# Kernel optimization log

Hardware: AMD Instinct MI355X
Metric: run time of the kernel (lower is better)

Reference implementation:

```python
import jax, jax.numpy as jnp
import numpy as np

N = 50000
E = 800000
IN_FEATS = 128
OUT_FEATS = 64
ALPHA = 0.2  # LeakyReLU negative slope


def setup_inputs() -> dict:
    key = jax.random.key(0)
    k1, k2, k3, k4, k5 = jax.random.split(key, 5)
    h = jax.random.normal(k1, (N, IN_FEATS), dtype=jnp.float32)
    src = jax.random.randint(k2, (E,), 0, N)
    dst = jax.random.randint(k3, (E,), 0, N)
    edge_index = jnp.stack([src, dst], axis=0).astype(jnp.int64)
    # xavier_uniform with gain=1.414
    limW = 1.414 * np.sqrt(6.0 / (IN_FEATS + OUT_FEATS))
    W = jax.random.uniform(k4, (IN_FEATS, OUT_FEATS), dtype=jnp.float32, minval=-limW, maxval=limW)
    lima = 1.414 * np.sqrt(6.0 / (2 * OUT_FEATS + 1))
    a = jax.random.uniform(k5, (2 * OUT_FEATS, 1), dtype=jnp.float32, minval=-lima, maxval=lima)
    return {"h": h, "edge_index": edge_index, "W": W, "a": a}


def reference(h, edge_index, W, a):
    src, dst = edge_index[0], edge_index[1]
    Wh = h @ W                               # (N, out)
    # split attention vector: cat([Wh_src, Wh_dst]) @ a == Wh_src@a1 + Wh_dst@a2
    a1 = a[:OUT_FEATS, 0]                    # (out,)
    a2 = a[OUT_FEATS:, 0]                    # (out,)
    s1 = Wh @ a1                             # (N,)
    s2 = Wh @ a2                             # (N,)
    e = jax.nn.leaky_relu(s1[src] + s2[dst], negative_slope=ALPHA)  # (E,)
    exp_e = jnp.exp(e)
    denom = jax.ops.segment_sum(exp_e, dst, num_segments=N)          # (N,)
    attention = exp_e / denom[dst]                                   # (E,)
    # dropout p=0.0 / eval mode -> identity
    msgs = attention[:, None] * Wh[src]                              # (E, out)
    h_prime = jax.ops.segment_sum(msgs, dst, num_segments=N)         # (N, out)
    return jax.nn.elu(h_prime)
```

## Files before the change

### kernel.cpp

```cpp
#include <hip/hip_runtime.h>
#include <math.h>

#define GN 50000
#define GE 800000
#define INF 128
#define OUTF 64
#define LRELU_ALPHA 0.2f

#define BUCK_SH 6
#define BUCKW   64
#define NB      ((GN + BUCKW - 1) / BUCKW)
#define CHUNK   4096
#define NCH     ((GE + CHUNK - 1) / CHUNK)
#define CAP     1536

__device__ __forceinline__ unsigned short f32_to_bf16(float f) {
    unsigned int u = __float_as_uint(f);
    return (unsigned short)((u + 0x7fffu + ((u >> 16) & 1u)) >> 16);
}
__device__ __forceinline__ float bf16lo(unsigned int u) { return __uint_as_float(u << 16); }
__device__ __forceinline__ float bf16hi(unsigned int u) { return __uint_as_float(u & 0xffff0000u); }

__global__ __launch_bounds__(256) void k_front(const float* __restrict__ h,
                                               const float* __restrict__ W,
                                               const float* __restrict__ a,
                                               const int* __restrict__ src,
                                               const int* __restrict__ dst,
                                               unsigned short* __restrict__ Whb,
                                               float* __restrict__ s1,
                                               float* __restrict__ s2,
                                               int* __restrict__ ccount,
                                               int* __restrict__ epacked) {
    __shared__ __align__(16) float Wlds[INF * OUTF];
    int t = threadIdx.x;

    if (blockIdx.x < NB) {
        for (int i = t * 4; i < INF * OUTF; i += 256 * 4)
            *(float4*)&Wlds[i] = *(const float4*)&W[i];
        __syncthreads();

        int fg = t & 15;
        int ng = t >> 4;
        int jg = fg * 4;
        int n0 = blockIdx.x * 64 + ng * 4;

        int m0 = n0 + 0 < GN ? n0 + 0 : GN - 1;
        int m1 = n0 + 1 < GN ? n0 + 1 : GN - 1;
        int m2 = n0 + 2 < GN ? n0 + 2 : GN - 1;
        int m3 = n0 + 3 < GN ? n0 + 3 : GN - 1;
        const float* h0 = &h[m0 * INF];
        const float* h1 = &h[m1 * INF];
        const float* h2 = &h[m2 * INF];
        const float* h3 = &h[m3 * INF];

        float4 acc0 = {0.f,0.f,0.f,0.f}, acc1 = acc0, acc2 = acc0, acc3 = acc0;
        for (int kc = 0; kc < INF; kc += 4) {
            float4 hv0 = *(const float4*)&h0[kc];
            float4 hv1 = *(const float4*)&h1[kc];
            float4 hv2 = *(const float4*)&h2[kc];
            float4 hv3 = *(const float4*)&h3[kc];
            #pragma unroll
            for (int kk = 0; kk < 4; ++kk) {
                float4 wv = *(float4*)&Wlds[(kc + kk) * OUTF + jg];
                float a0 = ((const float*)&hv0)[kk];
                float a1v = ((const float*)&hv1)[kk];
                float a2v = ((const float*)&hv2)[kk];
                float a3 = ((const float*)&hv3)[kk];
                acc0.x += a0 * wv.x; acc0.y += a0 * wv.y; acc0.z += a0 * wv.z; acc0.w += a0 * wv.w;
                acc1.x += a1v * wv.x; acc1.y += a1v * wv.y; acc1.z += a1v * wv.z; acc1.w += a1v * wv.w;
                acc2.x += a2v * wv.x; acc2.y += a2v * wv.y; acc2.z += a2v * wv.z; acc2.w += a2v * wv.w;
                acc3.x += a3 * wv.x; acc3.y += a3 * wv.y; acc3.z += a3 * wv.z; acc3.w += a3 * wv.w;
            }
        }

        float4 accs[4] = {acc0, acc1, acc2, acc3};
        #pragma unroll
        for (int i = 0; i < 4; ++i) {
            if (n0 + i < GN) {
                ushort4 p;
                p.x = f32_to_bf16(accs[i].x); p.y = f32_to_bf16(accs[i].y);
                p.z = f32_to_bf16(accs[i].z); p.w = f32_to_bf16(accs[i].w);
                *(ushort4*)&Whb[(n0 + i) * OUTF + jg] = p;
            }
        }

        float4 va1 = *(const float4*)&a[jg];
        float4 va2 = *(const float4*)&a[OUTF + jg];
        float p1[4], p2[4];
        #pragma unroll
        for (int i = 0; i < 4; ++i) {
            p1[i] = accs[i].x * va1.x + accs[i].y * va1.y + accs[i].z * va1.z + accs[i].w * va1.w;
            p2[i] = accs[i].x * va2.x + accs[i].y * va2.y + accs[i].z * va2.z + accs[i].w * va2.w;
        }
        #pragma unroll
        for (int off = 8; off >= 1; off >>= 1) {
            #pragma unroll
            for (int i = 0; i < 4; ++i) {
                p1[i] += __shfl_down(p1[i], off, 16);
                p2[i] += __shfl_down(p2[i], off, 16);
            }
        }
        if (fg == 0) {
            #pragma unroll
            for (int i = 0; i < 4; ++i) {
                if (n0 + i < GN) { s1[n0 + i] = p1[i]; s2[n0 + i] = p2[i]; }
            }
        }
    } else {
        int* hist = (int*)Wlds;
        int* run  = hist + NB;
        for (int i = t; i < NB; i += 256) hist[i] = 0;
        __syncthreads();

        int base = (blockIdx.x - NB) * CHUNK;
        int pk[CHUNK / 256];
        int bb[CHUNK / 256];
        #pragma unroll
        for (int i = 0; i < CHUNK / 256; ++i) {
            int e = base + i * 256 + t;
            if (e < GE) {
                int d = dst[e];
                int b = d >> BUCK_SH;
                pk[i] = (src[e] << BUCK_SH) | (d & (BUCKW - 1));
                bb[i] = b;
                atomicAdd(&hist[b], 1);
            } else {
                bb[i] = -1;
            }
        }
        __syncthreads();
        for (int i = t; i < NB; i += 256) {
            int c = hist[i];
            if (c > 0) run[i] = i * CAP + atomicAdd(&ccount[i], c);
        }
        __syncthreads();
        #pragma unroll
        for (int i = 0; i < CHUNK / 256; ++i) {
            if (bb[i] >= 0) {
                int pos = atomicAdd(&run[bb[i]], 1);
                epacked[pos] = pk[i];
            }
        }
    }
}

__global__ __launch_bounds__(256) void k_fgather(const int* __restrict__ ccount,
                                                 const int* __restrict__ epacked,
                                                 const float* __restrict__ s1,
                                                 const float* __restrict__ s2,
                                                 const unsigned short* __restrict__ Whb,
                                                 float* __restrict__ out) {
    __shared__ int elds[CAP];
    __shared__ int sorted[CAP];
    __shared__ int hist[BUCKW];
    __shared__ int cur[BUCKW];
    __shared__ int cstart[BUCKW + 1];
    __shared__ float s2l[BUCKW];

    int t = threadIdx.x;
    int b = blockIdx.x;
    int dstbase = b * BUCKW;
    int nd = GN - dstbase; if (nd > BUCKW) nd = BUCKW;

    int start = b * CAP;
    int cnt   = ccount[b];
    if (cnt > CAP) cnt = CAP;

    if (t < BUCKW) {
        hist[t] = 0;
        s2l[t] = (t < nd) ? s2[dstbase + t] : 0.f;
    }
    __syncthreads();
    for (int i = t; i < cnt; i += 256) {
        int pk = epacked[start + i];
        elds[i] = pk;
        atomicAdd(&hist[pk & (BUCKW - 1)], 1);
    }
    __syncthreads();
    if (t < 64) {
        int v = hist[t];
        int incl = v;
        #pragma unroll
        for (int off = 1; off < 64; off <<= 1) {
            int u = __shfl_up(incl, off, 64);
            if (t >= off) incl += u;
        }
        cstart[t + 1] = incl;
        cur[t] = incl - v;
        if (t == 0) cstart[0] = 0;
    }
    __syncthreads();
    for (int i = t; i < cnt; i += 256) {
        int pk = elds[i];
        int pos = atomicAdd(&cur[pk & (BUCKW - 1)], 1);
        sorted[pos] = pk;
    }
    __syncthreads();

    int grp  = t >> 3;
    int lane = t & 7;
    int jg   = lane * 8;
    for (int dl = grp; dl < BUCKW; dl += 32) {
        int c0 = cstart[dl], c1 = cstart[dl + 1];
        float acc[8] = {0.f,0.f,0.f,0.f,0.f,0.f,0.f,0.f};
        float den = 0.f;
        float s2n = s2l[dl];
        for (int cb = c0; cb < c1; cb += 8) {
            int my = cb + lane;
            float ex_l = 0.f; int s_l = 0;
            if (my < c1) {
                int pk = sorted[my];
                s_l = pk >> BUCK_SH;
                float x = s1[s_l] + s2n;
                x = (x > 0.f) ? x : LRELU_ALPHA * x;
                ex_l = expf(x);
            }
            int m = c1 - cb; if (m > 8) m = 8;
            int   sj[8]; float exj[8];
            #pragma unroll
            for (int j = 0; j < 8; ++j) {
                exj[j] = __shfl(ex_l, j, 8);
                sj[j]  = __shfl(s_l,  j, 8);
            }
            uint4 wv[8];
            #pragma unroll
            for (int j = 0; j < 8; ++j)
                if (j < m) wv[j] = *(const uint4*)&Whb[sj[j] * OUTF + jg];
            #pragma unroll
            for (int j = 0; j < 8; ++j) {
                if (j < m) {
                    float ex = exj[j];
                    den += ex;
                    acc[0] += ex * bf16lo(wv[j].x); acc[1] += ex * bf16hi(wv[j].x);
                    acc[2] += ex * bf16lo(wv[j].y); acc[3] += ex * bf16hi(wv[j].y);
                    acc[4] += ex * bf16lo(wv[j].z); acc[5] += ex * bf16hi(wv[j].z);
                    acc[6] += ex * bf16lo(wv[j].w); acc[7] += ex * bf16hi(wv[j].w);
                }
            }
        }
        if (dl < nd) {
            float inv = (c1 > c0) ? 1.f / den : 0.f;
            float o[8];
            #pragma unroll
            for (int j = 0; j < 8; ++j) {
                float v = acc[j] * inv;
                o[j] = (v > 0.f) ? v : expm1f(v);
            }
            float* op = &out[(dstbase + dl) * OUTF + jg];
            *(float4*)(op + 0) = make_float4(o[0], o[1], o[2], o[3]);
            *(float4*)(op + 4) = make_float4(o[4], o[5], o[6], o[7]);
        }
    }
}

extern "C" void kernel_launch(void* const* d_in, const int* in_sizes, int n_in,
                              void* d_out, int out_size, void* d_ws, size_t ws_size,
                              hipStream_t stream) {
    const float* h  = (const float*)d_in[0];
    const int*   ei = (const int*)d_in[1];
    const float* W  = (const float*)d_in[2];
    const float* a  = (const float*)d_in[3];
    const int* src = ei;
    const int* dst = ei + GE;

    float* ws = (float*)d_ws;
    float* s1 = ws;
    float* s2 = s1 + GN;
    unsigned short* Whb = (unsigned short*)(s2 + GN);
    int* epacked = (int*)(Whb + (size_t)GN * OUTF);
    int* ccount  = epacked + (size_t)NB * CAP;
    float* out = (float*)d_out;

    hipMemsetAsync(ccount, 0, NB * sizeof(int), stream);
    k_front<<<NB + NCH, 256, 0, stream>>>(h, W, a, src, dst, Whb, s1, s2,
                                          ccount, epacked);
    k_fgather<<<NB, 256, 0, stream>>>(ccount, epacked, s1, s2, Whb, out);
}
```

Baseline: 131.1 us.

## Split each gather bucket across two blocks, one 32-destination half each

The gather kernel now launches two blocks per 64-destination bucket. Each block filters the bucket's edges down to its own 32-destination half, reading epacked twice from global memory instead of staging it in LDS. Each 8-thread group then handles exactly one destination. This doubles the block count and halves LDS use to raise occupancy and parallelism, at the cost of redundant edge reads and histogram passes. It also switches expf to the faster __expf intrinsic and caps each half at HCAP=1024 edges, which could drop edges if a half overflows.

Result: no change. 132.2 us (+0.8%).

```diff
diff --git a/kernel.cpp b/kernel.cpp
--- a/kernel.cpp
+++ b/kernel.cpp
@@ -11,8 +11,9 @@
 #define BUCKW   64
 #define NB      ((GN + BUCKW - 1) / BUCKW)
 #define CHUNK   4096
-#define NCH     ((GE + CHUNK - 1) / CHUNK)
+#define NCH     ((GE + CHUNK - 1) / GE * 0 + (GE + CHUNK - 1) / CHUNK)
 #define CAP     1536
+#define HCAP    1024
 
 __device__ __forceinline__ unsigned short f32_to_bf16(float f) {
     unsigned int u = __float_as_uint(f);
@@ -150,39 +151,39 @@
                                                  const float* __restrict__ s2,
                                                  const unsigned short* __restrict__ Whb,
                                                  float* __restrict__ out) {
-    __shared__ int elds[CAP];
-    __shared__ int sorted[CAP];
-    __shared__ int hist[BUCKW];
-    __shared__ int cur[BUCKW];
-    __shared__ int cstart[BUCKW + 1];
-    __shared__ float s2l[BUCKW];
-
-    int t = threadIdx.x;
-    int b = blockIdx.x;
-    int dstbase = b * BUCKW;
-    int nd = GN - dstbase; if (nd > BUCKW) nd = BUCKW;
+    __shared__ int sorted[HCAP];
+    __shared__ int hist[32];
+    __shared__ int cur[32];
+    __shared__ int cstart[33];
+    __shared__ float s2l[32];
+
+    int t  = threadIdx.x;
+    int b  = blockIdx.x >> 1;
+    int fh = blockIdx.x & 1;
+    int dstbase = b * BUCKW + fh * 32;
+    int nd = GN - dstbase;
+    if (nd < 0) nd = 0; if (nd > 32) nd = 32;
 
     int start = b * CAP;
     int cnt   = ccount[b];
     if (cnt > CAP) cnt = CAP;
 
-    if (t < BUCKW) {
+    if (t < 32) {
         hist[t] = 0;
         s2l[t] = (t < nd) ? s2[dstbase + t] : 0.f;
     }
     __syncthreads();
     for (int i = t; i < cnt; i += 256) {
-        int pk = epacked[start + i];
-        elds[i] = pk;
-        atomicAdd(&hist[pk & (BUCKW - 1)], 1);
-    }
-    __syncthreads();
-    if (t < 64) {
+        int dl = epacked[start + i] & (BUCKW - 1);
+        if ((dl >> 5) == fh) atomicAdd(&hist[dl & 31], 1);
+    }
+    __syncthreads();
+    if (t < 32) {
         int v = hist[t];
         int incl = v;
         #pragma unroll
-        for (int off = 1; off < 64; off <<= 1) {
-            int u = __shfl_up(incl, off, 64);
+        for (int off = 1; off < 32; off <<= 1) {
+            int u = __shfl_up(incl, off, 32);
             if (t >= off) incl += u;
         }
         cstart[t + 1] = incl;
@@ -191,65 +192,68 @@
     }
     __syncthreads();
     for (int i = t; i < cnt; i += 256) {
-        int pk = elds[i];
-        int pos = atomicAdd(&cur[pk & (BUCKW - 1)], 1);
-        sorted[pos] = pk;
+        int pk = epacked[start + i];
+        int dl = pk & (BUCKW - 1);
+        if ((dl >> 5) == fh) {
+            int pos = atomicAdd(&cur[dl & 31], 1);
+            if (pos < HCAP) sorted[pos] = pk;
+        }
     }
     __syncthreads();
 
     int grp  = t >> 3;
     int lane = t & 7;
     int jg   = lane * 8;
-    for (int dl = grp; dl < BUCKW; dl += 32) {
-        int c0 = cstart[dl], c1 = cstart[dl + 1];
-        float acc[8] = {0.f,0.f,0.f,0.f,0.f,0.f,0.f,0.f};
-        float den = 0.f;
-        float s2n = s2l[dl];
-        for (int cb = c0; cb < c1; cb += 8) {
-            int my = cb + lane;
-            float ex_l = 0.f; int s_l = 0;
-            if (my < c1) {
-                int pk = sorted[my];
-                s_l = pk >> BUCK_SH;
-                float x = s1[s_l] + s2n;
-                x = (x > 0.f) ? x : LRELU_ALPHA * x;
-                ex_l = expf(x);
-            }
-            int m = c1 - cb; if (m > 8) m = 8;
-            int   sj[8]; float exj[8];
-            #pragma unroll
-            for (int j = 0; j < 8; ++j) {
-                exj[j] = __shfl(ex_l, j, 8);
-                sj[j]  = __shfl(s_l,  j, 8);
-            }
-            uint4 wv[8];
-            #pragma unroll
-            for (int j = 0; j < 8; ++j)
-                if (j < m) wv[j] = *(const uint4*)&Whb[sj[j] * OUTF + jg];
-            #pragma unroll
-            for (int j = 0; j < 8; ++j) {
-                if (j < m) {
-                    float ex = exj[j];
-                    den += ex;
-                    acc[0] += ex * bf16lo(wv[j].x); acc[1] += ex * bf16hi(wv[j].x);
-                    acc[2] += ex * bf16lo(wv[j].y); acc[3] += ex * bf16hi(wv[j].y);
-                    acc[4] += ex * bf16lo(wv[j].z); acc[5] += ex * bf16hi(wv[j].z);
-                    acc[6] += ex * bf16lo(wv[j].w); acc[7] += ex * bf16hi(wv[j].w);
-                }
-            }
-        }
-        if (dl < nd) {
-            float inv = (c1 > c0) ? 1.f / den : 0.f;
-            float o[8];
-            #pragma unroll
-            for (int j = 0; j < 8; ++j) {
-                float v = acc[j] * inv;
-                o[j] = (v > 0.f) ? v : expm1f(v);
-            }
-            float* op = &out[(dstbase + dl) * OUTF + jg];
-            *(float4*)(op + 0) = make_float4(o[0], o[1], o[2], o[3]);
-            *(float4*)(op + 4) = make_float4(o[4], o[5], o[6], o[7]);
-        }
+    int c0 = cstart[grp];
+    int c1 = cstart[grp + 1];
+    if (c1 > HCAP) c1 = HCAP;
+    float acc[8] = {0.f,0.f,0.f,0.f,0.f,0.f,0.f,0.f};
+    float den = 0.f;
+    float s2n = s2l[grp];
+    for (int cb = c0; cb < c1; cb += 8) {
+        int my = cb + lane;
+        float ex_l = 0.f; int s_l = 0;
+        if (my < c1) {
+            int pk = sorted[my];
+            s_l = pk >> BUCK_SH;
+            float x = s1[s_l] + s2n;
+            x = (x > 0.f) ? x : LRELU_ALPHA * x;
+            ex_l = __expf(x);
+        }
+        int m = c1 - cb; if (m > 8) m = 8;
+        int   sj[8]; float exj[8];
+        #pragma unroll
+        for (int j = 0; j < 8; ++j) {
+            exj[j] = __shfl(ex_l, j, 8);
+            sj[j]  = __shfl(s_l,  j, 8);
+        }
+        uint4 wv[8];
+        #pragma unroll
+        for (int j = 0; j < 8; ++j)
+            if (j < m) wv[j] = *(const uint4*)&Whb[sj[j] * OUTF + jg];
+        #pragma unroll
+        for (int j = 0; j < 8; ++j) {
+            if (j < m) {
+                float ex = exj[j];
+                den += ex;
+                acc[0] += ex * bf16lo(wv[j].x); acc[1] += ex * bf16hi(wv[j].x);
+                acc[2] += ex * bf16lo(wv[j].y); acc[3] += ex * bf16hi(wv[j].y);
+                acc[4] += ex * bf16lo(wv[j].z); acc[5] += ex * bf16hi(wv[j].z);
+                acc[6] += ex * bf16lo(wv[j].w); acc[7] += ex * bf16hi(wv[j].w);
+            }
+        }
+    }
+    if (grp < nd) {
+        float inv = (c1 > c0) ? 1.f / den : 0.f;
+        float o[8];
+        #pragma unroll
+        for (int j = 0; j < 8; ++j) {
+            float v = acc[j] * inv;
+            o[j] = (v > 0.f) ? v : expm1f(v);
+        }
+        float* op = &out[(dstbase + grp) * OUTF + jg];
+        *(float4*)(op + 0) = make_float4(o[0], o[1], o[2], o[3]);
+        *(float4*)(op + 4) = make_float4(o[4], o[5], o[6], o[7]);
     }
 }
 
@@ -274,5 +278,5 @@
     hipMemsetAsync(ccount, 0, NB * sizeof(int), stream);
     k_front<<<NB + NCH, 256, 0, stream>>>(h, W, a, src, dst, Whb, s1, s2,
                                           ccount, epacked);
-    k_fgather<<<NB, 256, 0, stream>>>(ccount, epacked, s1, s2, Whb, out);
-}
+    k_fgather<<<NB * 2, 256, 0, stream>>>(ccount, epacked, s1, s2, Whb, out);
+}
```

## Fuse front and gather kernels into one persistent cooperative kernel with grid syncs

Applied to the files above, without the earlier changes.

Replaces the memset and two kernel launches with a single cooperative persistent kernel. It zeroes counters, runs the GEMM and edge-bucketing tasks, grid-syncs, then runs the per-bucket gather. Buckets shrink from 64 to 49 destinations (NB=1021, CAP=1024) via a multiply-shift divide, and expf becomes __expf. This aims to remove launch gaps and match the bucket count to the grid size, at the cost of grid-sync overhead and a smaller per-bucket capacity that could overflow and drop edges.

Result: slower. 325.7 us (+148.4%).

```diff
diff --git a/kernel.cpp b/kernel.cpp
--- a/kernel.cpp
+++ b/kernel.cpp
@@ -1,5 +1,8 @@
 #include <hip/hip_runtime.h>
+#include <hip/hip_cooperative_groups.h>
 #include <math.h>
+
+namespace cg = cooperative_groups;
 
 #define GN 50000
 #define GE 800000
@@ -7,12 +10,17 @@
 #define OUTF 64
 #define LRELU_ALPHA 0.2f
 
-#define BUCK_SH 6
-#define BUCKW   64
-#define NB      ((GN + BUCKW - 1) / BUCKW)
+#define BUCKW   49
+#define NB      1021
+#define CAP     1024
 #define CHUNK   4096
 #define NCH     ((GE + CHUNK - 1) / CHUNK)
-#define CAP     1536
+#define NGT     782
+#define NT1     (NGT + NCH)
+
+__device__ __forceinline__ unsigned div49(unsigned d) {
+    return (d * 85599u) >> 22;
+}
 
 __device__ __forceinline__ unsigned short f32_to_bf16(float f) {
     unsigned int u = __float_as_uint(f);
@@ -21,235 +29,241 @@
 __device__ __forceinline__ float bf16lo(unsigned int u) { return __uint_as_float(u << 16); }
 __device__ __forceinline__ float bf16hi(unsigned int u) { return __uint_as_float(u & 0xffff0000u); }
 
-__global__ __launch_bounds__(256) void k_front(const float* __restrict__ h,
-                                               const float* __restrict__ W,
-                                               const float* __restrict__ a,
-                                               const int* __restrict__ src,
-                                               const int* __restrict__ dst,
-                                               unsigned short* __restrict__ Whb,
-                                               float* __restrict__ s1,
-                                               float* __restrict__ s2,
-                                               int* __restrict__ ccount,
-                                               int* __restrict__ epacked) {
-    __shared__ __align__(16) float Wlds[INF * OUTF];
+__global__ __launch_bounds__(256, 4)
+void k_all(const float* __restrict__ h,
+           const float* __restrict__ W,
+           const float* __restrict__ a,
+           const int* __restrict__ src,
+           const int* __restrict__ dst,
+           unsigned short* __restrict__ Whb,
+           float* __restrict__ s1,
+           float* __restrict__ s2,
+           int* __restrict__ ccount,
+           int* __restrict__ epacked,
+           float* __restrict__ out) {
+    __shared__ __align__(16) unsigned char smem[32768];
     int t = threadIdx.x;
-
-    if (blockIdx.x < NB) {
-        for (int i = t * 4; i < INF * OUTF; i += 256 * 4)
-            *(float4*)&Wlds[i] = *(const float4*)&W[i];
-        __syncthreads();
-
-        int fg = t & 15;
-        int ng = t >> 4;
-        int jg = fg * 4;
-        int n0 = blockIdx.x * 64 + ng * 4;
-
-        int m0 = n0 + 0 < GN ? n0 + 0 : GN - 1;
-        int m1 = n0 + 1 < GN ? n0 + 1 : GN - 1;
-        int m2 = n0 + 2 < GN ? n0 + 2 : GN - 1;
-        int m3 = n0 + 3 < GN ? n0 + 3 : GN - 1;
-        const float* h0 = &h[m0 * INF];
-        const float* h1 = &h[m1 * INF];
-        const float* h2 = &h[m2 * INF];
-        const float* h3 = &h[m3 * INF];
-
-        float4 acc0 = {0.f,0.f,0.f,0.f}, acc1 = acc0, acc2 = acc0, acc3 = acc0;
-        for (int kc = 0; kc < INF; kc += 4) {
-            float4 hv0 = *(const float4*)&h0[kc];
-            float4 hv1 = *(const float4*)&h1[kc];
-            float4 hv2 = *(const float4*)&h2[kc];
-            float4 hv3 = *(const float4*)&h3[kc];
-            #pragma unroll
-            for (int kk = 0; kk < 4; ++kk) {
-                float4 wv = *(float4*)&Wlds[(kc + kk) * OUTF + jg];
-                float a0 = ((const float*)&hv0)[kk];
-                float a1v = ((const float*)&hv1)[kk];
-                float a2v = ((const float*)&hv2)[kk];
-                float a3 = ((const float*)&hv3)[kk];
-                acc0.x += a0 * wv.x; acc0.y += a0 * wv.y; acc0.z += a0 * wv.z; acc0.w += a0 * wv.w;
-                acc1.x += a1v * wv.x; acc1.y += a1v * wv.y; acc1.z += a1v * wv.z; acc1.w += a1v * wv.w;
-                acc2.x += a2v * wv.x; acc2.y += a2v * wv.y; acc2.z += a2v * wv.z; acc2.w += a2v * wv.w;
-                acc3.x += a3 * wv.x; acc3.y += a3 * wv.y; acc3.z += a3 * wv.z; acc3.w += a3 * wv.w;
-            }
-        }
-
-        float4 accs[4] = {acc0, acc1, acc2, acc3};
-        #pragma unroll
-        for (int i = 0; i < 4; ++i) {
-            if (n0 + i < GN) {
-                ushort4 p;
-                p.x = f32_to_bf16(accs[i].x); p.y = f32_to_bf16(accs[i].y);
-                p.z = f32_to_bf16(accs[i].z); p.w = f32_to_bf16(accs[i].w);
-                *(ushort4*)&Whb[(n0 + i) * OUTF + jg] = p;
-            }
-        }
-
-        float4 va1 = *(const float4*)&a[jg];
-        float4 va2 = *(const float4*)&a[OUTF + jg];
-        float p1[4], p2[4];
-        #pragma unroll
-        for (int i = 0; i < 4; ++i) {
-            p1[i] = accs[i].x * va1.x + accs[i].y * va1.y + accs[i].z * va1.z + accs[i].w * va1.w;
-            p2[i] = accs[i].x * va2.x + accs[i].y * va2.y + accs[i].z * va2.z + accs[i].w * va2.w;
-        }
-        #pragma unroll
-        for (int off = 8; off >= 1; off >>= 1) {
+    int grid = gridDim.x;
+    cg::grid_group gg = cg::this_grid();
+
+    for (int i = blockIdx.x * 256 + t; i < NB; i += grid * 256) ccount[i] = 0;
+    gg.sync();
+
+    for (int task = blockIdx.x; task < NT1; task += grid) {
+        if (task < NGT) {
+            float* Wlds = (float*)smem;
+            for (int i = t * 4; i < INF * OUTF; i += 256 * 4)
+                *(float4*)&Wlds[i] = *(const float4*)&W[i];
+            __syncthreads();
+
+            int fg = t & 15;
+            int ng = t >> 4;
+            int jg = fg * 4;
+            int n0 = task * 64 + ng * 4;
+
+            int m0 = n0 + 0 < GN ? n0 + 0 : GN - 1;
+            int m1 = n0 + 1 < GN ? n0 + 1 : GN - 1;
+            int m2 = n0 + 2 < GN ? n0 + 2 : GN - 1;
+            int m3 = n0 + 3 < GN ? n0 + 3 : GN - 1;
+            const float* h0 = &h[m0 * INF];
+            const float* h1 = &h[m1 * INF];
+            const float* h2 = &h[m2 * INF];
+            const float* h3 = &h[m3 * INF];
+
+            float4 acc0 = {0.f,0.f,0.f,0.f}, acc1 = acc0, acc2 = acc0, acc3 = acc0;
+            for (int kc = 0; kc < INF; kc += 4) {
+                float4 hv0 = *(const float4*)&h0[kc];
+                float4 hv1 = *(const float4*)&h1[kc];
+                float4 hv2 = *(const float4*)&h2[kc];
+                float4 hv3 = *(const float4*)&h3[kc];
+                #pragma unroll
+                for (int kk = 0; kk < 4; ++kk) {
+                    float4 wv = *(float4*)&Wlds[(kc + kk) * OUTF + jg];
+                    float a0 = ((const float*)&hv0)[kk];
+                    float a1v = ((const float*)&hv1)[kk];
+                    float a2v = ((const float*)&hv2)[kk];
+                    float a3 = ((const float*)&hv3)[kk];
+                    acc0.x += a0 * wv.x; acc0.y += a0 * wv.y; acc0.z += a0 * wv.z; acc0.w += a0 * wv.w;
+                    acc1.x += a1v * wv.x; acc1.y += a1v * wv.y; acc1.z += a1v * wv.z; acc1.w += a1v * wv.w;
+                    acc2.x += a2v * wv.x; acc2.y += a2v * wv.y; acc2.z += a2v * wv.z; acc2.w += a2v * wv.w;
+                    acc3.x += a3 * wv.x; acc3.y += a3 * wv.y; acc3.z += a3 * wv.z; acc3.w += a3 * wv.w;
+                }
+            }
+
+            float4 accs[4] = {acc0, acc1, acc2, acc3};
             #pragma unroll
             for (int i = 0; i < 4; ++i) {
-                p1[i] += __shfl_down(p1[i], off, 16);
-                p2[i] += __shfl_down(p2[i], off, 16);
-            }
-        }
-        if (fg == 0) {
+                if (n0 + i < GN) {
+                    ushort4 p;
+                    p.x = f32_to_bf16(accs[i].x); p.y = f32_to_bf16(accs[i].y);
+                    p.z = f32_to_bf16(accs[i].z); p.w = f32_to_bf16(accs[i].w);
+                    *(ushort4*)&Whb[(n0 + i) * OUTF + jg] = p;
+                }
+            }
+
+            float4 va1 = *(const float4*)&a[jg];
+            float4 va2 = *(const float4*)&a[OUTF + jg];
+            float p1[4], p2[4];
             #pragma unroll
             for (int i = 0; i < 4; ++i) {
-                if (n0 + i < GN) { s1[n0 + i] = p1[i]; s2[n0 + i] = p2[i]; }
-            }
-        }
-    } else {
-        int* hist = (int*)Wlds;
-        int* run  = hist + NB;
-        for (int i = t; i < NB; i += 256) hist[i] = 0;
-        __syncthreads();
-
-        int base = (blockIdx.x - NB) * CHUNK;
-        int pk[CHUNK / 256];
-        int bb[CHUNK / 256];
-        #pragma unroll
-        for (int i = 0; i < CHUNK / 256; ++i) {
-            int e = base + i * 256 + t;
-            if (e < GE) {
-                int d = dst[e];
-                int b = d >> BUCK_SH;
-                pk[i] = (src[e] << BUCK_SH) | (d & (BUCKW - 1));
-                bb[i] = b;
-                atomicAdd(&hist[b], 1);
-            } else {
-                bb[i] = -1;
-            }
-        }
-        __syncthreads();
-        for (int i = t; i < NB; i += 256) {
-            int c = hist[i];
-            if (c > 0) run[i] = i * CAP + atomicAdd(&ccount[i], c);
-        }
-        __syncthreads();
-        #pragma unroll
-        for (int i = 0; i < CHUNK / 256; ++i) {
-            if (bb[i] >= 0) {
-                int pos = atomicAdd(&run[bb[i]], 1);
-                epacked[pos] = pk[i];
-            }
-        }
+                p1[i] = accs[i].x * va1.x + accs[i].y * va1.y + accs[i].z * va1.z + accs[i].w * va1.w;
+                p2[i] = accs[i].x * va2.x + accs[i].y * va2.y + accs[i].z * va2.z + accs[i].w * va2.w;
+            }
+            #pragma unroll
+            for (int off = 8; off >= 1; off >>= 1) {
+                #pragma unroll
+                for (int i = 0; i < 4; ++i) {
+                    p1[i] += __shfl_down(p1[i], off, 16);
+                    p2[i] += __shfl_down(p2[i], off, 16);
+                }
+            }
+            if (fg == 0) {
+                #pragma unroll
+                for (int i = 0; i < 4; ++i) {
+                    if (n0 + i < GN) { s1[n0 + i] = p1[i]; s2[n0 + i] = p2[i]; }
+                }
+            }
+        } else {
+            int* hist = (int*)smem;
+            int* run  = hist + NB;
+            for (int i = t; i < NB; i += 256) hist[i] = 0;
+            __syncthreads();
+
+            int base = (task - NGT) * CHUNK;
+            int pk[CHUNK / 256];
+            int bb[CHUNK / 256];
+            #pragma unroll
+            for (int i = 0; i < CHUNK / 256; ++i) {
+                int e = base + i * 256 + t;
+                if (e < GE) {
+                    unsigned d = (unsigned)dst[e];
+                    unsigned b = div49(d);
+                    pk[i] = (src[e] << 6) | (int)(d - b * BUCKW);
+                    bb[i] = (int)b;
+                    atomicAdd(&hist[b], 1);
+                } else {
+                    bb[i] = -1;
+                }
+            }
+            __syncthreads();
+            for (int i = t; i < NB; i += 256) {
+                int c = hist[i];
+                if (c > 0) run[i] = i * CAP + atomicAdd(&ccount[i], c);
+            }
+            __syncthreads();
+            #pragma unroll
+            for (int i = 0; i < CHUNK / 256; ++i) {
+                if (bb[i] >= 0) {
+                    int pos = atomicAdd(&run[bb[i]], 1);
+                    epacked[pos] = pk[i];
+                }
+            }
+        }
+        __syncthreads();
     }
-}
-
-__global__ __launch_bounds__(256) void k_fgather(const int* __restrict__ ccount,
-                                                 const int* __restrict__ epacked,
-                                                 const float* __restrict__ s1,
-                                                 const float* __restrict__ s2,
-                                                 const unsigned short* __restrict__ Whb,
-                                                 float* __restrict__ out) {
-    __shared__ int elds[CAP];
-    __shared__ int sorted[CAP];
-    __shared__ int hist[BUCKW];
-    __shared__ int cur[BUCKW];
-    __shared__ int cstart[BUCKW + 1];
-    __shared__ float s2l[BUCKW];
-
-    int t = threadIdx.x;
-    int b = blockIdx.x;
-    int dstbase = b * BUCKW;
-    int nd = GN - dstbase; if (nd > BUCKW) nd = BUCKW;
-
-    int start = b * CAP;
-    int cnt   = ccount[b];
-    if (cnt > CAP) cnt = CAP;
-
-    if (t < BUCKW) {
-        hist[t] = 0;
-        s2l[t] = (t < nd) ? s2[dstbase + t] : 0.f;
-    }
-    __syncthreads();
-    for (int i = t; i < cnt; i += 256) {
-        int pk = epacked[start + i];
-        elds[i] = pk;
-        atomicAdd(&hist[pk & (BUCKW - 1)], 1);
-    }
-    __syncthreads();
-    if (t < 64) {
-        int v = hist[t];
-        int incl = v;
-        #pragma unroll
-        for (int off = 1; off < 64; off <<= 1) {
-            int u = __shfl_up(incl, off, 64);
-            if (t >= off) incl += u;
-        }
-        cstart[t + 1] = incl;
-        cur[t] = incl - v;
-        if (t == 0) cstart[0] = 0;
-    }
-    __syncthreads();
-    for (int i = t; i < cnt; i += 256) {
-        int pk = elds[i];
-        int pos = atomicAdd(&cur[pk & (BUCKW - 1)], 1);
-        sorted[pos] = pk;
-    }
-    __syncthreads();
-
-    int grp  = t >> 3;
-    int lane = t & 7;
-    int jg   = lane * 8;
-    for (int dl = grp; dl < BUCKW; dl += 32) {
-        int c0 = cstart[dl], c1 = cstart[dl + 1];
-        float acc[8] = {0.f,0.f,0.f,0.f,0.f,0.f,0.f,0.f};
-        float den = 0.f;
-        float s2n = s2l[dl];
-        for (int cb = c0; cb < c1; cb += 8) {
-            int my = cb + lane;
-            float ex_l = 0.f; int s_l = 0;
-            if (my < c1) {
-                int pk = sorted[my];
-                s_l = pk >> BUCK_SH;
-                float x = s1[s_l] + s2n;
-                x = (x > 0.f) ? x : LRELU_ALPHA * x;
-                ex_l = expf(x);
-            }
-            int m = c1 - cb; if (m > 8) m = 8;
-            int   sj[8]; float exj[8];
-            #pragma unroll
-            for (int j = 0; j < 8; ++j) {
-                exj[j] = __shfl(ex_l, j, 8);
-                sj[j]  = __shfl(s_l,  j, 8);
-            }
-            uint4 wv[8];
-            #pragma unroll
-            for (int j = 0; j < 8; ++j)
-                if (j < m) wv[j] = *(const uint4*)&Whb[sj[j] * OUTF + jg];
-            #pragma unroll
-            for (int j = 0; j < 8; ++j) {
-                if (j < m) {
-                    float ex = exj[j];
-                    den += ex;
-                    acc[0] += ex * bf16lo(wv[j].x); acc[1] += ex * bf16hi(wv[j].x);
-                    acc[2] += ex * bf16lo(wv[j].y); acc[3] += ex * bf16hi(wv[j].y);
-                    acc[4] += ex * bf16lo(wv[j].z); acc[5] += ex * bf16hi(wv[j].z);
-                    acc[6] += ex * bf16lo(wv[j].w); acc[7] += ex * bf16hi(wv[j].w);
-                }
-            }
-        }
-        if (dl < nd) {
-            float inv = (c1 > c0) ? 1.f / den : 0.f;
-            float o[8];
-            #pragma unroll
-            for (int j = 0; j < 8; ++j) {
-                float v = acc[j] * inv;
-                o[j] = (v > 0.f) ? v : expm1f(v);
-            }
-            float* op = &out[(dstbase + dl) * OUTF + jg];
-            *(float4*)(op + 0) = make_float4(o[0], o[1], o[2], o[3]);
-            *(float4*)(op + 4) = make_float4(o[4], o[5], o[6], o[7]);
-        }
+    __threadfence();
+    gg.sync();
+
+    int* elds   = (int*)smem;
+    int* sorted = elds + CAP;
+    int* hist   = sorted + CAP;
+    int* cur    = hist + 64;
+    int* cstart = cur + 64;
+    float* s2l  = (float*)(cstart + 66);
+
+    for (int b = blockIdx.x; b < NB; b += grid) {
+        int dstbase = b * BUCKW;
+        int nd = GN - dstbase;
+        if (nd < 0) nd = 0; if (nd > BUCKW) nd = BUCKW;
+
+        int start = b * CAP;
+        int cnt = ccount[b];
+        if (cnt > CAP) cnt = CAP;
+
+        if (t < 64) hist[t] = 0;
+        if (t < BUCKW) s2l[t] = (t < nd) ? s2[dstbase + t] : 0.f;
+        __syncthreads();
+        for (int i = t; i < cnt; i += 256) {
+            int pk = epacked[start + i];
+            elds[i] = pk;
+            atomicAdd(&hist[pk & 63], 1);
+        }
+        __syncthreads();
+        if (t < 64) {
+            int v = hist[t];
+            int incl = v;
+            #pragma unroll
+            for (int off = 1; off < 64; off <<= 1) {
+                int u = __shfl_up(incl, off, 64);
+                if (t >= off) incl += u;
+            }
+            cstart[t + 1] = incl;
+            cur[t] = incl - v;
+            if (t == 0) cstart[0] = 0;
+        }
+        __syncthreads();
+        for (int i = t; i < cnt; i += 256) {
+            int pk = elds[i];
+            int pos = atomicAdd(&cur[pk & 63], 1);
+            sorted[pos] = pk;
+        }
+        __syncthreads();
+
+        int grp  = t >> 3;
+        int lane = t & 7;
+        int jg   = lane * 8;
+        for (int dl = grp; dl < BUCKW; dl += 32) {
+            int c0 = cstart[dl], c1 = cstart[dl + 1];
+            float acc[8] = {0.f,0.f,0.f,0.f,0.f,0.f,0.f,0.f};
+            float den = 0.f;
+            float s2n = s2l[dl];
+            for (int cb = c0; cb < c1; cb += 8) {
+                int my = cb + lane;
+                float ex_l = 0.f; int s_l = 0;
+                if (my < c1) {
+                    int pk = sorted[my];
+                    s_l = pk >> 6;
+                    float x = s1[s_l] + s2n;
+                    x = (x > 0.f) ? x : LRELU_ALPHA * x;
+                    ex_l = __expf(x);
+                }
+                int m = c1 - cb; if (m > 8) m = 8;
+                int   sj[8]; float exj[8];
+                #pragma unroll
+                for (int j = 0; j < 8; ++j) {
+                    exj[j] = __shfl(ex_l, j, 8);
+                    sj[j]  = __shfl(s_l,  j, 8);
+                }
+                uint4 wv[8];
+                #pragma unroll
+                for (int j = 0; j < 8; ++j)
+                    if (j < m) wv[j] = *(const uint4*)&Whb[sj[j] * OUTF + jg];
+                #pragma unroll
+                for (int j = 0; j < 8; ++j) {
+                    if (j < m) {
+                        float ex = exj[j];
+                        den += ex;
+                        acc[0] += ex * bf16lo(wv[j].x); acc[1] += ex * bf16hi(wv[j].x);
+                        acc[2] += ex * bf16lo(wv[j].y); acc[3] += ex * bf16hi(wv[j].y);
+                        acc[4] += ex * bf16lo(wv[j].z); acc[5] += ex * bf16hi(wv[j].z);
+                        acc[6] += ex * bf16lo(wv[j].w); acc[7] += ex * bf16hi(wv[j].w);
+                    }
+                }
+            }
+            if (dl < nd) {
+                float inv = (c1 > c0) ? 1.f / den : 0.f;
+                float o[8];
+                #pragma unroll
+                for (int j = 0; j < 8; ++j) {
+                    float v = acc[j] * inv;
+                    o[j] = (v > 0.f) ? v : expm1f(v);
+                }
+                float* op = &out[(dstbase + dl) * OUTF + jg];
+                *(float4*)(op + 0) = make_float4(o[0], o[1], o[2], o[3]);
+                *(float4*)(op + 4) = make_float4(o[4], o[5], o[6], o[7]);
+            }
+        }
+        __syncthreads();
     }
 }
 
@@ -271,8 +285,15 @@
     int* ccount  = epacked + (size_t)NB * CAP;
     float* out = (float*)d_out;
 
-    hipMemsetAsync(ccount, 0, NB * sizeof(int), stream);
-    k_front<<<NB + NCH, 256, 0, stream>>>(h, W, a, src, dst, Whb, s1, s2,
-                                          ccount, epacked);
-    k_fgather<<<NB, 256, 0, stream>>>(ccount, epacked, s1, s2, Whb, out);
-}
+    int occ = 0;
+    hipOccupancyMaxActiveBlocksPerMultiprocessor(&occ, (const void*)k_all, 256, 0);
+    if (occ < 1) occ = 1;
+    int grid = occ * 256;
+    if (grid > 1024) grid = 1024;
+
+    void* args[] = {(void*)&h, (void*)&W, (void*)&a, (void*)&src, (void*)&dst,
+                    (void*)&Whb, (void*)&s1, (void*)&s2, (void*)&ccount,
+                    (void*)&epacked, (void*)&out};
+    hipLaunchCooperativeKernel((const void*)k_all, dim3(grid), dim3(256),
+                               args, 0, stream);
+}
```
